# Performance work log

Measured on AMD Instinct MI355X. Metric: run time of the kernel, lower is better.

## Reference

```python
import jax, jax.numpy as jnp
import numpy as np

ALPHA = 0.044194173824159216  # 1/sqrt(512)
EPS = 1e-6
C, G, HW = 512, 32, 4096


def setup_inputs() -> dict:
    key = jax.random.key(0)
    ks = jax.random.split(key, 10)
    s = 1.0 / np.sqrt(C)
    return {
        "x": jax.random.normal(ks[0], (8, C, 64, 64), dtype=jnp.float32),
        "gamma": jnp.ones((C,), jnp.float32),
        "beta": jnp.zeros((C,), jnp.float32),
        "wq": jax.random.uniform(ks[1], (C, C), jnp.float32, -s, s),
        "bq": jax.random.uniform(ks[2], (C,), jnp.float32, -s, s),
        "wk": jax.random.uniform(ks[3], (C, C), jnp.float32, -s, s),
        "bk": jax.random.uniform(ks[4], (C,), jnp.float32, -s, s),
        "wv": jax.random.uniform(ks[5], (C, C), jnp.float32, -s, s),
        "bv": jax.random.uniform(ks[6], (C,), jnp.float32, -s, s),
        "wo": jax.random.uniform(ks[7], (C, C), jnp.float32, -s, s),
        "bo": jax.random.uniform(ks[8], (C,), jnp.float32, -s, s),
    }


def _group_norm(x, gamma, beta):
    B = x.shape[0]
    xg = x.reshape(B, G, C // G, 64, 64)
    mu = jnp.mean(xg, axis=(2, 3, 4), keepdims=True)
    var = jnp.var(xg, axis=(2, 3, 4), keepdims=True)
    xn = ((xg - mu) / jnp.sqrt(var + EPS)).reshape(B, C, 64, 64)
    return xn * gamma[None, :, None, None] + beta[None, :, None, None]


def reference(x, gamma, beta, wq, bq, wk, bk, wv, bv, wo, bo):
    B = x.shape[0]
    res = x
    h = _group_norm(x, gamma, beta)
    # [B, HW, C]
    h = h.reshape(B, C, HW).transpose(0, 2, 1)
    q = h @ wq.T + bq
    k = h @ wk.T + bk
    v = h @ wv.T + bv
    # scores [B, HW, HW]
    scores = ALPHA * jnp.einsum("bnc,bmc->bnm", q, k)
    attn = jax.nn.softmax(scores, axis=2)
    o = jnp.einsum("bnm,bmc->bnc", attn, v)
    o = o @ wo.T + bo
    o = o.transpose(0, 2, 1).reshape(B, C, 64, 64)
    return o + res
```

## Files before the change

kernel.cpp:

```cpp
#include <hip/hip_runtime.h>
#include <hip/hip_bf16.h>

typedef __attribute__((ext_vector_type(8))) short short8;
typedef __attribute__((ext_vector_type(4))) float f32x4;

#define ALPHA 0.044194173824159216f

#define GLO(p) (const __attribute__((address_space(1))) void*)(p)
#define LDSP(p) (__attribute__((address_space(3))) void*)(p)

__device__ __forceinline__ unsigned short f2bf(float f) {
    union { float f; unsigned int u; } c; c.f = f;
    unsigned int u = c.u;
    return (unsigned short)((u + 0x7FFFu + ((u >> 16) & 1u)) >> 16);
}

__device__ __forceinline__ float bf2f(unsigned short s) {
    union { unsigned int u; float f; } c; c.u = ((unsigned int)s) << 16;
    return c.f;
}

__global__ __launch_bounds__(256) void gn_stats(const float* __restrict__ x,
                                                float* __restrict__ stats) {
    int blk = blockIdx.x;
    const float4* src = (const float4*)(x + (size_t)blk * 65536);
    float s = 0.f, sq = 0.f;
    for (int i = threadIdx.x; i < 16384; i += 256) {
        float4 v = src[i];
        s  += v.x + v.y + v.z + v.w;
        sq += v.x*v.x + v.y*v.y + v.z*v.z + v.w*v.w;
    }
    for (int off = 32; off; off >>= 1) {
        s  += __shfl_down(s, off);
        sq += __shfl_down(sq, off);
    }
    __shared__ float ss[4], ssq[4];
    int wid = threadIdx.x >> 6;
    if ((threadIdx.x & 63) == 0) { ss[wid] = s; ssq[wid] = sq; }
    __syncthreads();
    if (threadIdx.x == 0) {
        float S = ss[0]+ss[1]+ss[2]+ss[3], Q = ssq[0]+ssq[1]+ssq[2]+ssq[3];
        float mu = S * (1.f/65536.f);
        float var = Q * (1.f/65536.f) - mu*mu;
        stats[blk] = mu;
        stats[256 + blk] = rsqrtf(var + 1e-6f);
    }
}

__global__ __launch_bounds__(256) void wcvt(const float* __restrict__ s,
                                            unsigned short* __restrict__ d) {
    int i = blockIdx.x * 1024 + threadIdx.x * 4;
    float4 v = *(const float4*)(s + i);
    ushort4 o = make_ushort4(f2bf(v.x), f2bf(v.y), f2bf(v.z), f2bf(v.w));
    *(ushort4*)(d + i) = o;
}

__global__ __launch_bounds__(256) void zero_l(float* __restrict__ l) {
    ((float4*)l)[blockIdx.x * 256 + threadIdx.x] = make_float4(0.f, 0.f, 0.f, 0.f);
}

__global__ __launch_bounds__(256) void recip(float* __restrict__ l) {
    int i = blockIdx.x * 256 + threadIdx.x;
    float4 v = ((const float4*)l)[i];
    ((float4*)l)[i] = make_float4(1.f / v.x, 1.f / v.y, 1.f / v.z, 1.f / v.w);
}

__global__ __launch_bounds__(256) void gn_apply(const float* __restrict__ x,
                                                const float* __restrict__ stats,
                                                const float* __restrict__ gamma,
                                                const float* __restrict__ beta,
                                                unsigned short* __restrict__ h) {
    __shared__ unsigned short t[64][72];
    int b = blockIdx.z, c0 = blockIdx.y * 64, hw0 = blockIdx.x * 64;
    int tid = threadIdx.x;
#pragma unroll
    for (int rep = 0; rep < 4; ++rep) {
        int lin = rep * 256 + tid;
        int row = lin >> 4;
        int c4  = lin & 15;
        int c   = c0 + row;
        const float4* src = (const float4*)(x + ((size_t)(b*512 + c) << 12) + hw0);
        float4 v = src[c4];
        int sidx = b*32 + (c >> 4);
        float mu = stats[sidx], rs = stats[256 + sidx];
        float ga = gamma[c] * rs, be = beta[c] - mu * ga;
        t[c4*4+0][row] = f2bf(v.x * ga + be);
        t[c4*4+1][row] = f2bf(v.y * ga + be);
        t[c4*4+2][row] = f2bf(v.z * ga + be);
        t[c4*4+3][row] = f2bf(v.w * ga + be);
    }
    __syncthreads();
#pragma unroll
    for (int rep = 0; rep < 2; ++rep) {
        int lin = rep * 256 + tid;
        int row = lin >> 3;
        int u8  = lin & 7;
        unsigned short* dst = h + (((size_t)(b*4096 + hw0 + row)) << 9) + c0 + u8*8;
        *(short8*)dst = *(const short8*)&t[row][u8*8];
    }
}

__global__ __launch_bounds__(256, 2) void gemm_bt(const unsigned short* __restrict__ A,
                                                  int lda, long aZs,
                                                  const unsigned short* __restrict__ B,
                                                  int ldb, long bZs,
                                                  const float* __restrict__ bias,
                                                  const float* __restrict__ resid,
                                                  const float* __restrict__ lvec,
                                                  void* __restrict__ out,
                                                  long ldo, long oZs,
                                                  int K, int mode, float scale) {
    __shared__ unsigned short As[128][72], Bs[128][72];
    int z = blockIdx.z;
    A += (size_t)z * aZs;
    B += (size_t)z * bZs;
    unsigned short* outu = (unsigned short*)out + (size_t)z * oZs;
    int m0 = blockIdx.y * 128, n0 = blockIdx.x * 128;
    int tid = threadIdx.x, w = tid >> 6, l = tid & 63;
    int lr = l & 15, lq = l >> 4, lk = lq * 8;
    int rbase = (w >> 1) * 64, cbase = (w & 1) * 64;
    f32x4 acc[4][4] = {};
    for (int k0 = 0; k0 < K; k0 += 64) {
        __syncthreads();
#pragma unroll
        for (int p = 0; p < 4; ++p) {
            int lin = p * 256 + tid;
            int r = lin >> 3, qq = lin & 7;
            *(short8*)&As[r][qq*8] = *(const short8*)(A + (size_t)(m0 + r)*lda + k0 + qq*8);
            *(short8*)&Bs[r][qq*8] = *(const short8*)(B + (size_t)(n0 + r)*ldb + k0 + qq*8);
        }
        __syncthreads();
        short8 af[4][2], bfv[4][2];
#pragma unroll
        for (int i = 0; i < 4; ++i)
#pragma unroll
            for (int ks = 0; ks < 2; ++ks) {
                af[i][ks]  = *(const short8*)&As[rbase + i*16 + lr][ks*32 + lk];
                bfv[i][ks] = *(const short8*)&Bs[cbase + i*16 + lr][ks*32 + lk];
            }
#pragma unroll
        for (int ks = 0; ks < 2; ++ks)
#pragma unroll
            for (int i = 0; i < 4; ++i)
#pragma unroll
                for (int j = 0; j < 4; ++j)
                    acc[i][j] = __builtin_amdgcn_mfma_f32_16x16x32_bf16(af[i][ks], bfv[j][ks], acc[i][j], 0, 0, 0);
    }
    int lq4 = lq * 4;
    if (mode == 2) {
        float rlv[4];
#pragma unroll
        for (int j = 0; j < 4; ++j) rlv[j] = lvec[n0 + cbase + j*16 + lr];
        float* outf = (float*)out;
#pragma unroll
        for (int i = 0; i < 4; ++i) {
            int rowg = m0 + rbase + i*16 + lq4;
            float4 bq4 = *(const float4*)(bias + rowg);
            float bb[4] = {bq4.x, bq4.y, bq4.z, bq4.w};
            size_t ad[16];
            float lres[16];
#pragma unroll
            for (int j = 0; j < 4; ++j) {
                int colg = n0 + cbase + j*16 + lr;
                size_t base = ((size_t)(colg >> 12)) * 2097152 + (size_t)(colg & 4095);
#pragma unroll
                for (int r = 0; r < 4; ++r) {
                    ad[j*4+r] = base + (size_t)(rowg + r) * 4096;
                    lres[j*4+r] = resid[ad[j*4+r]];
                }
            }
#pragma unroll
            for (int j = 0; j < 4; ++j)
#pragma unroll
                for (int r = 0; r < 4; ++r)
                    outf[ad[j*4+r]] = acc[i][j][r] * rlv[j] + bb[r] + lres[j*4+r];
        }
        return;
    }
#pragma unroll
    for (int i = 0; i < 4; ++i) {
        int rowg = m0 + rbase + i*16 + lq4;
#pragma unroll
        for (int j = 0; j < 4; ++j) {
            int colg = n0 + cbase + j*16 + lr;
#pragma unroll
            for (int r = 0; r < 4; ++r) {
                float v = acc[i][j][r];
                int rr = rowg + r;
                if (mode == 0) {
                    outu[(size_t)rr * ldo + colg] = f2bf((v + bias[colg]) * scale);
                } else {
                    outu[(size_t)rr * ldo + colg] = f2bf(v + bias[rr]);
                }
            }
        }
    }
}

__device__ __forceinline__ void mm8_core(const unsigned short* __restrict__ A, int lda,
                                         const unsigned short* __restrict__ B, int ldb,
                                         int T,
                                         unsigned short (*As)[256][64],
                                         unsigned short (*Bs)[256][64],
                                         f32x4 acc[8][4]) {
    int tid = threadIdx.x, w = tid >> 6, l = tid & 63;
    int wr = w >> 2, wc = w & 3;
    int lr = l & 15, lq = l >> 4;
    int rsub = l >> 3, colp = ((l & 7) ^ rsub) << 3;
    int sw = (lr & 7) << 4;
    int aw = w * 8;

#define SG_A(buf, t_) { \
    const unsigned short* ap = A + (size_t)(t_) * 64; \
    __builtin_amdgcn_global_load_lds(GLO(ap + (size_t)(aw + rsub) * lda + colp),        LDSP(&As[buf][aw][0]), 16, 0, 0); \
    __builtin_amdgcn_global_load_lds(GLO(ap + (size_t)(64 + aw + rsub) * lda + colp),   LDSP(&As[buf][64 + aw][0]), 16, 0, 0); \
    __builtin_amdgcn_global_load_lds(GLO(ap + (size_t)(128 + aw + rsub) * lda + colp),  LDSP(&As[buf][128 + aw][0]), 16, 0, 0); \
    __builtin_amdgcn_global_load_lds(GLO(ap + (size_t)(192 + aw + rsub) * lda + colp),  LDSP(&As[buf][192 + aw][0]), 16, 0, 0); }
#define SG_B(buf, t_, h_) { \
    const unsigned short* bp = B + (size_t)(t_) * 64; int rb = (h_) * 128 + aw; \
    __builtin_amdgcn_global_load_lds(GLO(bp + (size_t)(rb + rsub) * ldb + colp),       LDSP(&Bs[buf][rb][0]), 16, 0, 0); \
    __builtin_amdgcn_global_load_lds(GLO(bp + (size_t)(rb + 64 + rsub) * ldb + colp),  LDSP(&Bs[buf][rb + 64][0]), 16, 0, 0); }
#define RD_B() { \
    const char* bsb = (const char*)Bs[cur]; \
    _Pragma("unroll") for (int nj = 0; nj < 4; ++nj) \
    _Pragma("unroll") for (int ks = 0; ks < 2; ++ks) { \
        int row = wc * 64 + nj * 16 + lr; \
        bf[nj][ks] = *(const short8*)(bsb + (((row << 7) + (ks << 6) + (lq << 4)) ^ sw)); } }
#define RD_A(p_) { \
    const char* asb = (const char*)As[cur]; \
    _Pragma("unroll") for (int i = 0; i < 2; ++i) \
    _Pragma("unroll") for (int ks = 0; ks < 2; ++ks) { \
        int row = wr * 128 + ((p_) * 2 + i) * 16 + lr; \
        af[i][ks] = *(const short8*)(asb + (((row << 7) + (ks << 6) + (lq << 4)) ^ sw)); } }
#define MM(p_) { \
    _Pragma("unroll") for (int ks = 0; ks < 2; ++ks) \
    _Pragma("unroll") for (int i = 0; i < 2; ++i) \
    _Pragma("unroll") for (int nj = 0; nj < 4; ++nj) \
        acc[(p_) * 2 + i][nj] = __builtin_amdgcn_mfma_f32_16x16x32_bf16(af[i][ks], bf[nj][ks], acc[(p_) * 2 + i][nj], 0, 0, 0); }
#define LGKM0 { asm volatile("s_waitcnt lgkmcnt(0)" ::: "memory"); __builtin_amdgcn_sched_barrier(0); }
#define VMC4 { asm volatile("s_waitcnt vmcnt(4)" ::: "memory"); __builtin_amdgcn_sched_barrier(0); }
#define VMC0 { asm volatile("s_waitcnt vmcnt(0)" ::: "memory"); __builtin_amdgcn_sched_barrier(0); }
#define BAR __builtin_amdgcn_s_barrier()

    SG_A(0, 0); SG_B(0, 0, 0); SG_B(0, 0, 1);
    if (T > 1) { SG_B(1, 1, 0); SG_B(1, 1, 1); VMC4; } else { VMC0; }
    BAR;
    for (int t = 0; t < T; ++t) {
        int cur = t & 1, nxt = cur ^ 1;
        short8 bf[4][2], af[2][2];
        RD_B(); RD_A(0);
        if (t + 1 < T) SG_A(nxt, t + 1);
        LGKM0; BAR;
        __builtin_amdgcn_s_setprio(1); MM(0); __builtin_amdgcn_s_setprio(0);
        BAR;
        RD_A(1);
        if (t + 2 < T) SG_B(cur, t + 2, 0);
        LGKM0; BAR;
        __builtin_amdgcn_s_setprio(1); MM(1); __builtin_amdgcn_s_setprio(0);
        BAR;
        RD_A(2);
        if (t + 2 < T) SG_B(cur, t + 2, 1);
        LGKM0; BAR;
        __builtin_amdgcn_s_setprio(1); MM(2); __builtin_amdgcn_s_setprio(0);
        BAR;
        RD_A(3);
        if (t + 2 < T) { VMC4; } else { VMC0; }
        LGKM0; BAR;
        __builtin_amdgcn_s_setprio(1); MM(3); __builtin_amdgcn_s_setprio(0);
        BAR;
    }
#undef SG_A
#undef SG_B
#undef RD_B
#undef RD_A
#undef MM
#undef LGKM0
#undef VMC4
#undef VMC0
#undef BAR
}

__global__ __launch_bounds__(512, 2) void s8(const unsigned short* __restrict__ q,
                                             const unsigned short* __restrict__ k,
                                             float* __restrict__ lout,
                                             unsigned short* __restrict__ P,
                                             int nwg) {
    __shared__ unsigned short As[2][256][64], Bs[2][256][64];
    int wk = (int)(blockIdx.x & 7) * (nwg >> 3) + (int)(blockIdx.x >> 3);
    int z = wk >> 8, rem = wk & 255;
    int m0 = (rem >> 4) << 8, n0 = (rem & 15) << 8;
    const unsigned short* A = q + (size_t)z * 2097152 + (size_t)m0 * 512;
    const unsigned short* B = k + (size_t)z * 2097152 + (size_t)n0 * 512;
    f32x4 acc[8][4] = {};
    mm8_core(A, 512, B, 512, 8, As, Bs, acc);
    unsigned short* Pz = P + (size_t)z * 16777216;
    float* lz = lout + z * 4096;
    int tid = threadIdx.x, w = tid >> 6, l = tid & 63;
    int wr = w >> 2, wc = w & 3, lr = l & 15, lq4 = (l >> 4) * 4;
#pragma unroll
    for (int mi = 0; mi < 8; ++mi) {
        int rowl = wr * 128 + mi * 16 + lq4;
#pragma unroll
        for (int r = 0; r < 4; ++r) {
            float s = 0.f;
#pragma unroll
            for (int nj = 0; nj < 4; ++nj) {
                float e = __expf(acc[mi][nj][r]);
                s += e;
                Pz[(size_t)(m0 + rowl + r) * 4096 + n0 + wc * 64 + nj * 16 + lr] = f2bf(e);
            }
            s += __shfl_xor(s, 1); s += __shfl_xor(s, 2);
            s += __shfl_xor(s, 4); s += __shfl_xor(s, 8);
            if (lr == 0) atomicAdd(&lz[m0 + rowl + r], s);
        }
    }
}

__global__ __launch_bounds__(512, 2) void pv8(const unsigned short* __restrict__ P0,
                                              const unsigned short* __restrict__ P1,
                                              const unsigned short* __restrict__ vt,
                                              unsigned short* __restrict__ part0,
                                              unsigned short* __restrict__ part1,
                                              int zofs, int nwg) {
    __shared__ unsigned short As[2][256][64], Bs[2][256][64];
    int wk = (int)(blockIdx.x & 7) * (nwg >> 3) + (int)(blockIdx.x >> 3);
    int half = nwg >> 1;
    int s = (wk >= half) ? 1 : 0;
    int rem = wk - s * half;
    int z = rem >> 5, t2 = rem & 31;
    int m0 = (t2 >> 1) << 8, n0 = (t2 & 1) << 8;
    const unsigned short* Pz = (z < 2) ? P0 + (size_t)z * 16777216
                                       : P1 + (size_t)(z - 2) * 16777216;
    const unsigned short* A = Pz + (size_t)m0 * 4096 + (size_t)s * 2048;
    const unsigned short* B = vt + (size_t)n0 * 32768 + (size_t)(zofs + z) * 4096 + (size_t)s * 2048;
    f32x4 acc[8][4] = {};
    mm8_core(A, 4096, B, 32768, 32, As, Bs, acc);
    unsigned short* pp = (s ? part1 : part0) + (size_t)z * 2097152 + (size_t)m0 * 512 + n0;
    int tid = threadIdx.x, w = tid >> 6, l = tid & 63;
    int wr = w >> 2, wc = w & 3, lr = l & 15, lq4 = (l >> 4) * 4;
#pragma unroll
    for (int mi = 0; mi < 8; ++mi)
#pragma unroll
        for (int nj = 0; nj < 4; ++nj)
#pragma unroll
            for (int r = 0; r < 4; ++r)
                pp[(size_t)(wr * 128 + mi * 16 + lq4 + r) * 512 + wc * 64 + nj * 16 + lr] = f2bf(acc[mi][nj][r]);
}

__global__ __launch_bounds__(256) void addcvt(const unsigned short* __restrict__ p0,
                                              const unsigned short* __restrict__ p1,
                                              unsigned short* __restrict__ o) {
    size_t i = ((size_t)blockIdx.x * 256 + threadIdx.x) * 8;
    short8 a = *(const short8*)(p0 + i), b = *(const short8*)(p1 + i);
    short8 r;
#pragma unroll
    for (int j = 0; j < 8; ++j)
        r[j] = (short)f2bf(bf2f((unsigned short)a[j]) + bf2f((unsigned short)b[j]));
    *(short8*)(o + i) = r;
}

extern "C" void kernel_launch(void* const* d_in, const int* in_sizes, int n_in,
                              void* d_out, int out_size, void* d_ws, size_t ws_size,
                              hipStream_t stream) {
    const float* x     = (const float*)d_in[0];
    const float* gamma = (const float*)d_in[1];
    const float* beta  = (const float*)d_in[2];
    const float* wq = (const float*)d_in[3];  const float* bq = (const float*)d_in[4];
    const float* wk = (const float*)d_in[5];  const float* bk = (const float*)d_in[6];
    const float* wv = (const float*)d_in[7];  const float* bv = (const float*)d_in[8];
    const float* wo = (const float*)d_in[9];  const float* bo = (const float*)d_in[10];

    char* wsp = (char*)d_ws;
    float* stats        = (float*)wsp;
    unsigned short* wqb = (unsigned short*)(wsp + 2048);
    unsigned short* wkb = wqb + 262144;
    unsigned short* wvb = wkb + 262144;
    unsigned short* wob = wvb + 262144;
    unsigned short* h   = wob + 262144;
    unsigned short* qb  = h  + 16777216;
    unsigned short* kb  = qb + 16777216;
    unsigned short* vtb = kb + 16777216;
    float* lbuf         = (float*)(vtb + 16777216);
    unsigned short* Pw  = (unsigned short*)(lbuf + 32768);
    unsigned short* Pd  = (unsigned short*)d_out;
    unsigned short* ob  = h;

    const bool mid = ws_size >= 204000000ull;

    gn_stats<<<256, 256, 0, stream>>>(x, stats);
    wcvt<<<256, 256, 0, stream>>>(wq, wqb);
    wcvt<<<256, 256, 0, stream>>>(wk, wkb);
    wcvt<<<256, 256, 0, stream>>>(wv, wvb);
    wcvt<<<256, 256, 0, stream>>>(wo, wob);
    gn_apply<<<dim3(64, 8, 8), 256, 0, stream>>>(x, stats, gamma, beta, h);
    zero_l<<<32, 256, 0, stream>>>(lbuf);

    gemm_bt<<<dim3(4, 256), 256, 0, stream>>>(h, 512, 0, wqb, 512, 0, bq, nullptr, nullptr,
                                              qb, 512, 0, 512, 0, ALPHA);
    gemm_bt<<<dim3(4, 256), 256, 0, stream>>>(h, 512, 0, wkb, 512, 0, bk, nullptr, nullptr,
                                              kb, 512, 0, 512, 0, 1.0f);
    gemm_bt<<<dim3(256, 4), 256, 0, stream>>>(wvb, 512, 0, h, 512, 0, bv, nullptr, nullptr,
                                              vtb, 32768, 0, 512, 1, 1.0f);

    const long QS = (long)4096 * 512;
    if (mid) {
        for (int c = 0; c < 2; ++c) {
            size_t z0 = (size_t)c * 4;
            s8<<<512, 512, 0, stream>>>(qb + z0 * QS, kb + z0 * QS,
                                        lbuf + z0 * 4096, Pd, 512);
            s8<<<512, 512, 0, stream>>>(qb + (z0 + 2) * QS, kb + (z0 + 2) * QS,
                                        lbuf + (z0 + 2) * 4096, Pw, 512);
            pv8<<<256, 512, 0, stream>>>(Pd, Pw, vtb,
                                         qb + z0 * QS, kb + z0 * QS, (int)z0, 256);
            addcvt<<<4096, 256, 0, stream>>>(qb + z0 * QS, kb + z0 * QS, ob + z0 * QS);
        }
    } else {
        for (int c = 0; c < 4; ++c) {
            size_t z0 = (size_t)c * 2;
            s8<<<512, 512, 0, stream>>>(qb + z0 * QS, kb + z0 * QS,
                                        lbuf + z0 * 4096, Pd, 512);
            pv8<<<128, 512, 0, stream>>>(Pd, Pd, vtb,
                                         qb + z0 * QS, kb + z0 * QS, (int)z0, 128);
            addcvt<<<2048, 256, 0, stream>>>(qb + z0 * QS, kb + z0 * QS, ob + z0 * QS);
        }
    }
    recip<<<32, 256, 0, stream>>>(lbuf);
    gemm_bt<<<dim3(256, 4), 256, 0, stream>>>(wob, 512, 0, ob, 512, 0, bo, x, lbuf,
                                              d_out, 0, 0, 512, 2, 1.0f);
}
```

Baseline: 780.0 us.

## Swap Q/K operands in score kernel for vectorized P stores and merge launches

The score kernel now computes K·Qᵀ tiles, so each lane's four accumulator values are contiguous along a P row. This lets it write packed ushort4 stores instead of scattered 2-byte stores, and reduce row sums across quad lanes. In mid mode the two per-chunk score launches are merged into one 1024-block launch that selects the P0/P1 buffer by batch index. The row-sum shuffle pattern and index mapping change, so correctness depends on the transposed layout matching what pv8 expects.

```diff
diff --git a/kernel.cpp b/kernel.cpp
--- a/kernel.cpp
+++ b/kernel.cpp
@@ -283,36 +283,42 @@
 __global__ __launch_bounds__(512, 2) void s8(const unsigned short* __restrict__ q,
                                              const unsigned short* __restrict__ k,
                                              float* __restrict__ lout,
-                                             unsigned short* __restrict__ P,
+                                             unsigned short* __restrict__ P0,
+                                             unsigned short* __restrict__ P1,
                                              int nwg) {
     __shared__ unsigned short As[2][256][64], Bs[2][256][64];
     int wk = (int)(blockIdx.x & 7) * (nwg >> 3) + (int)(blockIdx.x >> 3);
     int z = wk >> 8, rem = wk & 255;
     int m0 = (rem >> 4) << 8, n0 = (rem & 15) << 8;
-    const unsigned short* A = q + (size_t)z * 2097152 + (size_t)m0 * 512;
-    const unsigned short* B = k + (size_t)z * 2097152 + (size_t)n0 * 512;
+    const unsigned short* A = k + (size_t)z * 2097152 + (size_t)m0 * 512;
+    const unsigned short* B = q + (size_t)z * 2097152 + (size_t)n0 * 512;
     f32x4 acc[8][4] = {};
     mm8_core(A, 512, B, 512, 8, As, Bs, acc);
-    unsigned short* Pz = P + (size_t)z * 16777216;
+    unsigned short* Pz = (z < 2) ? P0 + (size_t)z * 16777216
+                                 : P1 + (size_t)(z - 2) * 16777216;
     float* lz = lout + z * 4096;
     int tid = threadIdx.x, w = tid >> 6, l = tid & 63;
-    int wr = w >> 2, wc = w & 3, lr = l & 15, lq4 = (l >> 4) * 4;
-#pragma unroll
-    for (int mi = 0; mi < 8; ++mi) {
-        int rowl = wr * 128 + mi * 16 + lq4;
-#pragma unroll
-        for (int r = 0; r < 4; ++r) {
-            float s = 0.f;
-#pragma unroll
-            for (int nj = 0; nj < 4; ++nj) {
-                float e = __expf(acc[mi][nj][r]);
-                s += e;
-                Pz[(size_t)(m0 + rowl + r) * 4096 + n0 + wc * 64 + nj * 16 + lr] = f2bf(e);
-            }
-            s += __shfl_xor(s, 1); s += __shfl_xor(s, 2);
-            s += __shfl_xor(s, 4); s += __shfl_xor(s, 8);
-            if (lr == 0) atomicAdd(&lz[m0 + rowl + r], s);
-        }
+    int wr = w >> 2, wc = w & 3, lr = l & 15, lq = l >> 4, lq4 = lq * 4;
+    int jb = m0 + wr * 128;
+    int ib = n0 + wc * 64;
+#pragma unroll
+    for (int nj = 0; nj < 4; ++nj) {
+        int i = ib + nj * 16 + lr;
+        unsigned short* prow = Pz + (size_t)i * 4096 + jb + lq4;
+        float rs = 0.f;
+#pragma unroll
+        for (int mi = 0; mi < 8; ++mi) {
+            float e0 = __expf(acc[mi][nj][0]);
+            float e1 = __expf(acc[mi][nj][1]);
+            float e2 = __expf(acc[mi][nj][2]);
+            float e3 = __expf(acc[mi][nj][3]);
+            rs += (e0 + e1) + (e2 + e3);
+            ushort4 pk = make_ushort4(f2bf(e0), f2bf(e1), f2bf(e2), f2bf(e3));
+            *(ushort4*)(prow + mi * 16) = pk;
+        }
+        rs += __shfl_xor(rs, 16);
+        rs += __shfl_xor(rs, 32);
+        if (lq == 0) atomicAdd(&lz[i], rs);
     }
 }
 
@@ -406,10 +412,8 @@
     if (mid) {
         for (int c = 0; c < 2; ++c) {
             size_t z0 = (size_t)c * 4;
-            s8<<<512, 512, 0, stream>>>(qb + z0 * QS, kb + z0 * QS,
-                                        lbuf + z0 * 4096, Pd, 512);
-            s8<<<512, 512, 0, stream>>>(qb + (z0 + 2) * QS, kb + (z0 + 2) * QS,
-                                        lbuf + (z0 + 2) * 4096, Pw, 512);
+            s8<<<1024, 512, 0, stream>>>(qb + z0 * QS, kb + z0 * QS,
+                                         lbuf + z0 * 4096, Pd, Pw, 1024);
             pv8<<<256, 512, 0, stream>>>(Pd, Pw, vtb,
                                          qb + z0 * QS, kb + z0 * QS, (int)z0, 256);
             addcvt<<<4096, 256, 0, stream>>>(qb + z0 * QS, kb + z0 * QS, ob + z0 * QS);
@@ -418,7 +422,7 @@
         for (int c = 0; c < 4; ++c) {
             size_t z0 = (size_t)c * 2;
             s8<<<512, 512, 0, stream>>>(qb + z0 * QS, kb + z0 * QS,
-                                        lbuf + z0 * 4096, Pd, 512);
+                                        lbuf + z0 * 4096, Pd, Pd, 512);
             pv8<<<128, 512, 0, stream>>>(Pd, Pd, vtb,
                                          qb + z0 * QS, kb + z0 * QS, (int)z0, 128);
             addcvt<<<2048, 256, 0, stream>>>(qb + z0 * QS, kb + z0 * QS, ob + z0 * QS);
```

Measured after the change: 724.6 us. 7.1% less time.
